# Kernel optimization log

Hardware: AMD Instinct MI355X
Metric: run time of the kernel (lower is better)

## Reference

```python
import jax, jax.numpy as jnp
import numpy as np
import math

B, H, L = 8, 512, 4096
N2 = 32  # d_state // 2


def setup_inputs() -> dict:
    key = jax.random.key(0)
    ks = jax.random.split(key, 8)
    u = jax.random.normal(ks[0], (B, H, L), dtype=jnp.float32)
    C = jax.random.normal(ks[1], (H, N2, 2), dtype=jnp.float32)  # view_as_real of cfloat C
    # log_dt ~ Uniform[log(dt_min), log(dt_max)], dt_min=1e-3, dt_max=0.1
    log_dt = jax.random.uniform(ks[2], (H,), dtype=jnp.float32,
                                minval=math.log(0.001), maxval=math.log(0.1))
    log_A_real = jnp.log(0.5 * jnp.ones((H, N2), dtype=jnp.float32))
    A_imag = math.pi * jnp.broadcast_to(jnp.arange(N2, dtype=jnp.float32), (H, N2))
    D = jax.random.normal(ks[3], (H,), dtype=jnp.float32)
    # pointwise Conv1d(H, 2H, kernel_size=1): weight (2H, H), bias (2H)
    fan = 1.0 / math.sqrt(H)
    W = jax.random.uniform(ks[4], (2 * H, H), dtype=jnp.float32, minval=-fan, maxval=fan)
    b = jax.random.uniform(ks[5], (2 * H,), dtype=jnp.float32, minval=-fan, maxval=fan)
    return {"u": u, "C": C, "log_dt": log_dt, "log_A_real": log_A_real,
            "A_imag": A_imag, "D": D, "W": W, "b": b}


def reference(u, C, log_dt, log_A_real, A_imag, D, W, b):
    Lb = u.shape[-1]
    # --- S4DKernel: kernel k of shape (H, L) ---
    dt = jnp.exp(log_dt)                                  # (H,)
    Cc = C[..., 0] + 1j * C[..., 1]                       # (H, N2) complex
    A = -jnp.exp(log_A_real) + 1j * A_imag                # (H, N2)
    dtA = A * dt[:, None]                                 # (H, N2)
    # Vandermonde: exp(dtA * l) for l in [0, L)
    K = jnp.exp(dtA[:, :, None] * jnp.arange(Lb, dtype=jnp.float32))  # (H, N2, L)
    Cmod = Cc * (jnp.exp(dtA) - 1.0) / A                  # (H, N2)
    k = 2.0 * jnp.einsum('hn,hnl->hl', Cmod, K).real      # (H, L)
    # --- FFT convolution (length 2L, causal) ---
    n = 2 * Lb
    k_f = jnp.fft.rfft(k, n=n)                            # (H, L+1)
    u_f = jnp.fft.rfft(u, n=n)                            # (B, H, L+1)
    y = jnp.fft.irfft(u_f * k_f, n=n)[..., :Lb]           # (B, H, L)
    # skip connection
    y = y + u * D[:, None]
    # activation (torch nn.GELU default = exact erf form)
    y = jax.nn.gelu(y, approximate=False)
    # pointwise conv (H -> 2H) + GLU over channel dim
    y = jnp.einsum('oh,bhl->bol', W, y) + b[None, :, None]  # (B, 2H, L)
    a, g = jnp.split(y, 2, axis=1)
    return a * jax.nn.sigmoid(g)                          # (B, H, L)
```

## Files before the change

### kernel.cpp

```cpp
#include <hip/hip_runtime.h>
#include <hip/hip_bf16.h>

constexpr int Bn = 8, Hn = 512, Ln = 4096, N2n = 32;

typedef _Float16 f16;
typedef __attribute__((ext_vector_type(8))) _Float16 f16x8;
typedef __attribute__((ext_vector_type(4))) _Float16 f16x4;
typedef __attribute__((ext_vector_type(2))) _Float16 f16x2;
typedef __attribute__((ext_vector_type(4))) float f32x4;

typedef void __attribute__((address_space(1))) gvoid;
typedef void __attribute__((address_space(3))) lvoid;

__global__ __launch_bounds__(64) void k_mats1(
    const float* __restrict__ C, const float* __restrict__ log_dt,
    const float* __restrict__ logA, const float* __restrict__ Aim,
    f16* __restrict__ Vg, f16* __restrict__ A3g, float2* __restrict__ w64g) {
  __shared__ f16 VT[64 * 64];
  __shared__ f16 QT[64 * 64];
  __shared__ float kp[64][33];
  __shared__ float ks[64];
  const int h = blockIdx.x, tid = threadIdx.x, n = tid & 31;

  if (tid < 32) {
    const int idx = h * N2n + n;
    float dt = expf(log_dt[h]);
    float Ar = -expf(logA[idx]);
    float Ai = Aim[idx];
    float dr = Ar * dt, di = Ai * dt;
    float er = expf(dr);
    float wr = er * cosf(di), wi = er * sinf(di);
    float den = Ar * Ar + Ai * Ai;
    float e1r = wr - 1.0f, e1i = wi;
    float tr = (e1r * Ar + e1i * Ai) / den;
    float ti = (e1i * Ar - e1r * Ai) / den;
    float Cr = C[idx * 2 + 0], Ci = C[idx * 2 + 1];
    float c2r = 2.0f * (Cr * tr - Ci * ti);
    float c2i = 2.0f * (Cr * ti + Ci * tr);

    float wpr = 1.f, wpi = 0.f;
    for (int p = 0; p <= 64; ++p) {
      float cwr = c2r * wpr - c2i * wpi;
      float cwi = c2r * wpi + c2i * wpr;
      if (p < 64) {
        const int j = 63 - p, ch = j >> 3, jo = j & 7;
        const int s0 = 2 * n, s1 = 2 * n + 1;
        VT[s0 * 64 + ((ch ^ (s0 & 7)) * 8) + jo] = (f16)wpr;
        VT[s1 * 64 + ((ch ^ (s1 & 7)) * 8) + jo] = (f16)wpi;
        kp[p][n] = cwr;
      }
      if (p >= 1) {
        const int t = p - 1, c0 = 2 * n;
        const int ch = (c0 >> 3) ^ (t & 7);
        QT[t * 64 + ch * 8 + (c0 & 7)]     = (f16)cwr;
        QT[t * 64 + ch * 8 + (c0 & 7) + 1] = (f16)(-cwi);
      }
      if (p == 64) w64g[h * 32 + n] = make_float2(wpr, wpi);
      float nr = wpr * wr - wpi * wi;
      float ni = wpr * wi + wpi * wr;
      wpr = nr; wpi = ni;
    }
  }
  __syncthreads();
  float s = 0.f;
#pragma unroll
  for (int m = 0; m < 32; ++m) s += kp[tid][m];
  ks[tid] = s;
  __syncthreads();
  const int t = tid;
#pragma unroll
  for (int c = 0; c < 8; ++c) {
    f16x8 row;
#pragma unroll
    for (int jo = 0; jo < 8; ++jo) {
      int j = c * 8 + jo;
      row[jo] = (j <= t) ? (f16)ks[t - j] : (f16)0.f;
    }
    *(f16x8*)&A3g[(size_t)h * 8192 + t * 128 + ((c ^ (t & 7)) * 8)] = row;
  }
#pragma unroll
  for (int c = 0; c < 8; ++c)
    *(f16x8*)&Vg[(size_t)h * 4096 + tid * 64 + c * 8] = *(f16x8*)&VT[tid * 64 + c * 8];
#pragma unroll
  for (int c = 0; c < 8; ++c)
    *(f16x8*)&A3g[(size_t)h * 8192 + tid * 128 + 64 + c * 8] = *(f16x8*)&QT[tid * 64 + c * 8];
}

__global__ void conv_w(const float* __restrict__ W, f16* __restrict__ Wh) {
  int i = blockIdx.x * 256 + threadIdx.x;
  if (i < 2 * Hn * Hn) Wh[i] = (f16)W[i];
}

__global__ __launch_bounds__(256, 1) void s4d_mid(
    const float* __restrict__ u, const f16* __restrict__ Vg,
    const f16* __restrict__ A3g, const float2* __restrict__ w64g,
    const float* __restrict__ Dv, f16* __restrict__ yg) {
  __shared__ f16 MATS[8192];
  __shared__ f16 U[32768];
  __shared__ f16 LE[32768];
  const int tid = threadIdx.x, wid = tid >> 6, lane = tid & 63;
  const int h = blockIdx.x;
  const float Dh = Dv[h];

#pragma unroll
  for (int q = 0; q < 2; ++q)
    __builtin_amdgcn_global_load_lds((const gvoid*)(Vg + (size_t)h * 4096 + (q * 256 + tid) * 8),
                                     (lvoid*)&MATS[(q * 256 + wid * 64) * 8], 16, 0, 0);
#pragma unroll
  for (int i = 0; i < 32; ++i) {
    int e = (i * 256 + tid) * 4;
    int b = e >> 12, l = e & 4095;
    float4 uv = *(const float4*)(u + ((size_t)(b * Hn + h)) * Ln + l);
    int col = b * 64 + (l >> 6), j = l & 63;
    f16x4 hv = {(f16)uv.x, (f16)uv.y, (f16)uv.z, (f16)uv.w};
    *(f16x4*)&U[col * 64 + ((j >> 3) ^ (col & 7)) * 8 + (j & 7)] = hv;
  }
  asm volatile("s_waitcnt vmcnt(0)" ::: "memory");
  __syncthreads();

  f32x4 acc[4][8];
#pragma unroll
  for (int i = 0; i < 4; ++i)
#pragma unroll
    for (int j = 0; j < 8; ++j) acc[i][j] = (f32x4){0.f, 0.f, 0.f, 0.f};
#pragma unroll
  for (int ks = 0; ks < 2; ++ks) {
    const int kc = ks * 4 + (lane >> 4);
    f16x8 a[4], bv[8];
#pragma unroll
    for (int mf = 0; mf < 4; ++mf) {
      int row = mf * 16 + (lane & 15);
      a[mf] = *(const f16x8*)&MATS[row * 64 + ((kc ^ (row & 7)) * 8)];
    }
#pragma unroll
    for (int nf = 0; nf < 8; ++nf) {
      int col = wid * 128 + nf * 16 + (lane & 15);
      bv[nf] = *(const f16x8*)&U[col * 64 + ((kc ^ (col & 7)) * 8)];
    }
#pragma unroll
    for (int mf = 0; mf < 4; ++mf)
#pragma unroll
      for (int nf = 0; nf < 8; ++nf)
        acc[mf][nf] = __builtin_amdgcn_mfma_f32_16x16x32_f16(a[mf], bv[nf], acc[mf][nf], 0, 0, 0);
  }
  __syncthreads();

#pragma unroll
  for (int q = 0; q < 4; ++q)
    __builtin_amdgcn_global_load_lds((const gvoid*)(A3g + (size_t)h * 8192 + (q * 256 + tid) * 8),
                                     (lvoid*)&MATS[(q * 256 + wid * 64) * 8], 16, 0, 0);

#pragma unroll
  for (int mf = 0; mf < 4; ++mf) {
    int st0 = mf * 16 + (lane >> 4) * 4;
#pragma unroll
    for (int nf = 0; nf < 8; ++nf) {
      int col = wid * 128 + nf * 16 + (lane & 15);
      f16x4 o = {(f16)acc[mf][nf][0], (f16)acc[mf][nf][1], (f16)acc[mf][nf][2], (f16)acc[mf][nf][3]};
      *(f16x4*)&LE[col * 64 + (((st0 >> 3) ^ (col & 7)) << 3) + (st0 & 7)] = o;
    }
  }
  __syncthreads();

  {
    const int b = tid >> 5, n = tid & 31;
    const float2 wT = w64g[h * 32 + n];
    float er = 0.f, ei = 0.f;
    const int inner = (((n >> 2)) << 3) + ((n & 3) << 1);
#pragma unroll
    for (int g = 0; g < 8; ++g) {
      f16x2 Lb[8];
#pragma unroll
      for (int k = 0; k < 8; ++k) {
        int blk = g * 8 + k;
        int col = b * 64 + blk;
        int fi = col * 64 + ((((n >> 2) ^ (blk & 7))) << 3) + ((n & 3) << 1);
        Lb[k] = *(const f16x2*)&LE[fi];
      }
#pragma unroll
      for (int k = 0; k < 8; ++k) {
        int blk = g * 8 + k;
        int col = b * 64 + blk;
        int fi = col * 64 + ((((n >> 2) ^ (blk & 7))) << 3) + ((n & 3) << 1);
        *(f16x2*)&LE[fi] = (f16x2){(f16)er, (f16)ei};
        float nr = fmaf(wT.x, er, fmaf(-wT.y, ei, (float)Lb[k][0]));
        float ni = fmaf(wT.y, er, fmaf(wT.x, ei, (float)Lb[k][1]));
        er = nr; ei = ni;
      }
    }
    (void)inner;
  }
  asm volatile("s_waitcnt vmcnt(0)" ::: "memory");
  __syncthreads();

  const int blk = wid * 16 + (lane & 15);
  for (int b = 0; b < 8; ++b) {
    const int col = b * 64 + blk;
    f32x4 acc4[4];
#pragma unroll
    for (int i = 0; i < 4; ++i) acc4[i] = (f32x4){0.f, 0.f, 0.f, 0.f};
#pragma unroll
    for (int ks = 0; ks < 4; ++ks) {
      const int kc = ks * 4 + (lane >> 4);
      f16x8 bf;
      if (ks < 2) bf = *(const f16x8*)&U[col * 64 + ((kc ^ (col & 7)) << 3)];
      else        bf = *(const f16x8*)&LE[col * 64 + (((kc - 8) ^ (col & 7)) << 3)];
#pragma unroll
      for (int mf = 0; mf < 4; ++mf) {
        int row = mf * 16 + (lane & 15);
        f16x8 af = *(const f16x8*)&MATS[row * 128 + ((kc ^ (row & 7)) << 3)];
        acc4[mf] = __builtin_amdgcn_mfma_f32_16x16x32_f16(af, bf, acc4[mf], 0, 0, 0);
      }
    }
    const int t0 = (lane >> 4) * 4;
#pragma unroll
    for (int mf = 0; mf < 4; ++mf) {
      const int tb = mf * 16 + t0;
      f16x4 uq = *(const f16x4*)&U[col * 64 + (((tb >> 3) ^ (col & 7)) << 3) + (tb & 7)];
      f16x4 o;
#pragma unroll
      for (int r = 0; r < 4; ++r) {
        float v = acc4[mf][r] + Dh * (float)uq[r];
        o[r] = (f16)(0.5f * v * (1.0f + erff(v * 0.70710678118654752f)));
      }
      *(f16x4*)&yg[((size_t)(b * Hn + h)) * Ln + blk * 64 + tb] = o;
    }
  }
}

__global__ __launch_bounds__(256) void k_transpose(
    const f16* __restrict__ yg, f16* __restrict__ gyT) {
  __shared__ float T[64][65];
  const int bid = blockIdx.x, tid = threadIdx.x;
  const int b = bid >> 9, hg = (bid >> 6) & 7, lg = bid & 63;
  const int h0 = hg * 64, l0 = lg * 64;
  const int hi = tid >> 2, lc = (tid & 3) * 16;
  const f16* src = yg + ((size_t)(b * Hn + h0 + hi)) * Ln + l0 + lc;
  f16x8 v0 = *(const f16x8*)src;
  f16x8 v1 = *(const f16x8*)(src + 8);
#pragma unroll
  for (int e = 0; e < 8; ++e) T[lc + e][hi] = (float)v0[e];
#pragma unroll
  for (int e = 0; e < 8; ++e) T[lc + 8 + e][hi] = (float)v1[e];
  __syncthreads();
  const int li = tid >> 2, hc = (tid & 3) * 16;
  f16x8 o0, o1;
#pragma unroll
  for (int e = 0; e < 8; ++e) o0[e] = (f16)T[li][hc + e];
#pragma unroll
  for (int e = 0; e < 8; ++e) o1[e] = (f16)T[li][hc + 8 + e];
  f16* dst = gyT + ((size_t)b * Ln + l0 + li) * Hn + h0 + hc;
  *(f16x8*)dst = o0;
  *(f16x8*)(dst + 8) = o1;
}

__global__ __launch_bounds__(256, 2) void s4d_gemm(
    const f16* __restrict__ Wh, const f16* __restrict__ gyT,
    const float* __restrict__ bias, float* __restrict__ out) {
  __shared__ f16 As[2][128][64];
  __shared__ f16 Bs[128][64];
  const int tid = threadIdx.x;
  const int wid = tid >> 6, lane = tid & 63;
  const int ntg = blockIdx.x & 255;
  const int mt = blockIdx.x >> 8;
  const int b = ntg >> 5;
  const int l0 = (ntg & 31) * 128;
  const int m0 = mt * 128;
  const int wm = wid >> 1, wn = wid & 1;

  f32x4 acc[2][4][4];
#pragma unroll
  for (int a = 0; a < 2; ++a)
#pragma unroll
    for (int i = 0; i < 4; ++i)
#pragma unroll
      for (int j = 0; j < 4; ++j) acc[a][i][j] = (f32x4){0.f, 0.f, 0.f, 0.f};

  const int srow = lane >> 3;
  const int sks = ((lane & 7) ^ srow) * 8;

  for (int kt = 0; kt < 8; ++kt) {
    const int k0 = kt * 64;
#pragma unroll
    for (int q = 0; q < 4; ++q) {
      const int r8 = wid * 32 + q * 8;
      const f16* srcA = Wh + ((size_t)(m0 + r8 + srow) * 512 + k0 + sks);
      __builtin_amdgcn_global_load_lds((const gvoid*)srcA, (lvoid*)&As[0][r8][0], 16, 0, 0);
      const f16* srcG = Wh + ((size_t)(Hn + m0 + r8 + srow) * 512 + k0 + sks);
      __builtin_amdgcn_global_load_lds((const gvoid*)srcG, (lvoid*)&As[1][r8][0], 16, 0, 0);
      const f16* srcB = gyT + (((size_t)b * Ln + l0 + r8 + srow) * Hn + k0 + sks);
      __builtin_amdgcn_global_load_lds((const gvoid*)srcB, (lvoid*)&Bs[r8][0], 16, 0, 0);
    }
    asm volatile("s_waitcnt vmcnt(0)" ::: "memory");
    __syncthreads();
#pragma unroll
    for (int kk = 0; kk < 2; ++kk) {
      const int kc = kk * 4 + (lane >> 4);
      f16x8 af0[4], af1[4], bfv[4];
#pragma unroll
      for (int mf = 0; mf < 4; ++mf) {
        const int row = wm * 64 + mf * 16 + (lane & 15);
        af0[mf] = *(const f16x8*)&As[0][row][(kc ^ (row & 7)) * 8];
        af1[mf] = *(const f16x8*)&As[1][row][(kc ^ (row & 7)) * 8];
      }
#pragma unroll
      for (int nf = 0; nf < 4; ++nf) {
        const int col = wn * 64 + nf * 16 + (lane & 15);
        bfv[nf] = *(const f16x8*)&Bs[col][(kc ^ (col & 7)) * 8];
      }
#pragma unroll
      for (int mf = 0; mf < 4; ++mf)
#pragma unroll
        for (int nf = 0; nf < 4; ++nf) {
          acc[0][mf][nf] = __builtin_amdgcn_mfma_f32_16x16x32_f16(af0[mf], bfv[nf], acc[0][mf][nf], 0, 0, 0);
          acc[1][mf][nf] = __builtin_amdgcn_mfma_f32_16x16x32_f16(af1[mf], bfv[nf], acc[1][mf][nf], 0, 0, 0);
        }
    }
    __syncthreads();
  }

  const int col = lane & 15, r0 = (lane >> 4) * 4;
#pragma unroll
  for (int mf = 0; mf < 4; ++mf) {
    const int hbase = m0 + wm * 64 + mf * 16 + r0;
#pragma unroll
    for (int nf = 0; nf < 4; ++nf) {
      const int l = l0 + wn * 64 + nf * 16 + col;
      f32x4 va = acc[0][mf][nf], vg = acc[1][mf][nf];
#pragma unroll
      for (int r = 0; r < 4; ++r) {
        const int hh = hbase + r;
        float av = va[r] + bias[hh];
        float gv = vg[r] + bias[Hn + hh];
        float sg = __builtin_amdgcn_rcpf(1.0f + __expf(-gv));
        out[((size_t)b * Hn + hh) * Ln + l] = av * sg;
      }
    }
  }
}

extern "C" void kernel_launch(void* const* d_in, const int* in_sizes, int n_in,
                              void* d_out, int out_size, void* d_ws, size_t ws_size,
                              hipStream_t stream) {
  (void)in_sizes; (void)n_in; (void)out_size; (void)ws_size;
  const float* u     = (const float*)d_in[0];
  const float* C     = (const float*)d_in[1];
  const float* logdt = (const float*)d_in[2];
  const float* logA  = (const float*)d_in[3];
  const float* Aim   = (const float*)d_in[4];
  const float* Dv    = (const float*)d_in[5];
  const float* W     = (const float*)d_in[6];
  const float* bias  = (const float*)d_in[7];
  float* out = (float*)d_out;

  char* ws = (char*)d_ws;
  f16*    gyT  = (f16*)ws;
  f16*    Vg   = (f16*)(ws + (size_t)(32 << 20));
  f16*    A3g  = (f16*)(ws + (size_t)(36 << 20));
  float2* w64g = (float2*)(ws + (size_t)(44 << 20));
  f16*    Wh   = (f16*)(ws + (size_t)(45 << 20));
  f16*    yg   = (f16*)d_out;

  hipLaunchKernelGGL(k_mats1, dim3(Hn), dim3(64), 0, stream, C, logdt, logA, Aim, Vg, A3g, w64g);
  hipLaunchKernelGGL(conv_w, dim3(2048), dim3(256), 0, stream, W, Wh);
  hipLaunchKernelGGL(s4d_mid, dim3(Hn), dim3(256), 0, stream, u, Vg, A3g, w64g, Dv, yg);
  hipLaunchKernelGGL(k_transpose, dim3(Bn * 8 * 64), dim3(256), 0, stream, yg, gyT);
  hipLaunchKernelGGL(s4d_gemm, dim3(4 * 256), dim3(256), 0, stream, Wh, gyT, bias, out);
}
```

Baseline: 120.4 us.

## Split s4d_mid grid across batch to shrink LDS and raise occupancy

The chunked scan kernel now launches one block per (head, batch) pair instead of one per head. Each block holds only one batch's 4096 samples, which cuts U/LE shared memory from 64 KB each to 8 KB each, and launch bounds now allow 4 blocks per CU. In exchange the per-head matrices (V, A3) are reloaded eight times. The inter-chunk recurrence also drops from 256 active threads to 32, which serialises that phase more within each block.

```diff
diff --git a/kernel.cpp b/kernel.cpp
--- a/kernel.cpp
+++ b/kernel.cpp
@@ -91,15 +91,15 @@
   if (i < 2 * Hn * Hn) Wh[i] = (f16)W[i];
 }
 
-__global__ __launch_bounds__(256, 1) void s4d_mid(
+__global__ __launch_bounds__(256, 4) void s4d_mid(
     const float* __restrict__ u, const f16* __restrict__ Vg,
     const f16* __restrict__ A3g, const float2* __restrict__ w64g,
     const float* __restrict__ Dv, f16* __restrict__ yg) {
   __shared__ f16 MATS[8192];
-  __shared__ f16 U[32768];
-  __shared__ f16 LE[32768];
+  __shared__ f16 U[4096];
+  __shared__ f16 LE[4096];
   const int tid = threadIdx.x, wid = tid >> 6, lane = tid & 63;
-  const int h = blockIdx.x;
+  const int h = blockIdx.x >> 3, b = blockIdx.x & 7;
   const float Dh = Dv[h];
 
 #pragma unroll
@@ -107,41 +107,30 @@
     __builtin_amdgcn_global_load_lds((const gvoid*)(Vg + (size_t)h * 4096 + (q * 256 + tid) * 8),
                                      (lvoid*)&MATS[(q * 256 + wid * 64) * 8], 16, 0, 0);
 #pragma unroll
-  for (int i = 0; i < 32; ++i) {
+  for (int i = 0; i < 4; ++i) {
     int e = (i * 256 + tid) * 4;
-    int b = e >> 12, l = e & 4095;
-    float4 uv = *(const float4*)(u + ((size_t)(b * Hn + h)) * Ln + l);
-    int col = b * 64 + (l >> 6), j = l & 63;
+    float4 uv = *(const float4*)(u + ((size_t)(b * Hn + h)) * Ln + e);
+    int col = e >> 6, j = e & 63;
     f16x4 hv = {(f16)uv.x, (f16)uv.y, (f16)uv.z, (f16)uv.w};
     *(f16x4*)&U[col * 64 + ((j >> 3) ^ (col & 7)) * 8 + (j & 7)] = hv;
   }
   asm volatile("s_waitcnt vmcnt(0)" ::: "memory");
   __syncthreads();
 
-  f32x4 acc[4][8];
-#pragma unroll
-  for (int i = 0; i < 4; ++i)
-#pragma unroll
-    for (int j = 0; j < 8; ++j) acc[i][j] = (f32x4){0.f, 0.f, 0.f, 0.f};
+  const int col = wid * 16 + (lane & 15);
+  f32x4 acc[4];
+#pragma unroll
+  for (int i = 0; i < 4; ++i) acc[i] = (f32x4){0.f, 0.f, 0.f, 0.f};
 #pragma unroll
   for (int ks = 0; ks < 2; ++ks) {
     const int kc = ks * 4 + (lane >> 4);
-    f16x8 a[4], bv[8];
+    f16x8 bv = *(const f16x8*)&U[col * 64 + ((kc ^ (col & 7)) * 8)];
 #pragma unroll
     for (int mf = 0; mf < 4; ++mf) {
       int row = mf * 16 + (lane & 15);
-      a[mf] = *(const f16x8*)&MATS[row * 64 + ((kc ^ (row & 7)) * 8)];
-    }
-#pragma unroll
-    for (int nf = 0; nf < 8; ++nf) {
-      int col = wid * 128 + nf * 16 + (lane & 15);
-      bv[nf] = *(const f16x8*)&U[col * 64 + ((kc ^ (col & 7)) * 8)];
-    }
-#pragma unroll
-    for (int mf = 0; mf < 4; ++mf)
-#pragma unroll
-      for (int nf = 0; nf < 8; ++nf)
-        acc[mf][nf] = __builtin_amdgcn_mfma_f32_16x16x32_f16(a[mf], bv[nf], acc[mf][nf], 0, 0, 0);
+      f16x8 a = *(const f16x8*)&MATS[row * 64 + ((kc ^ (row & 7)) * 8)];
+      acc[mf] = __builtin_amdgcn_mfma_f32_16x16x32_f16(a, bv, acc[mf], 0, 0, 0);
+    }
   }
   __syncthreads();
 
@@ -153,78 +142,66 @@
 #pragma unroll
   for (int mf = 0; mf < 4; ++mf) {
     int st0 = mf * 16 + (lane >> 4) * 4;
-#pragma unroll
-    for (int nf = 0; nf < 8; ++nf) {
-      int col = wid * 128 + nf * 16 + (lane & 15);
-      f16x4 o = {(f16)acc[mf][nf][0], (f16)acc[mf][nf][1], (f16)acc[mf][nf][2], (f16)acc[mf][nf][3]};
-      *(f16x4*)&LE[col * 64 + (((st0 >> 3) ^ (col & 7)) << 3) + (st0 & 7)] = o;
-    }
-  }
-  __syncthreads();
-
-  {
-    const int b = tid >> 5, n = tid & 31;
+    f16x4 o = {(f16)acc[mf][0], (f16)acc[mf][1], (f16)acc[mf][2], (f16)acc[mf][3]};
+    *(f16x4*)&LE[col * 64 + (((st0 >> 3) ^ (col & 7)) << 3) + (st0 & 7)] = o;
+  }
+  __syncthreads();
+
+  if (tid < 32) {
+    const int n = tid;
     const float2 wT = w64g[h * 32 + n];
     float er = 0.f, ei = 0.f;
-    const int inner = (((n >> 2)) << 3) + ((n & 3) << 1);
 #pragma unroll
     for (int g = 0; g < 8; ++g) {
       f16x2 Lb[8];
 #pragma unroll
       for (int k = 0; k < 8; ++k) {
         int blk = g * 8 + k;
-        int col = b * 64 + blk;
-        int fi = col * 64 + ((((n >> 2) ^ (blk & 7))) << 3) + ((n & 3) << 1);
+        int fi = blk * 64 + (((n >> 2) ^ (blk & 7)) << 3) + ((n & 3) << 1);
         Lb[k] = *(const f16x2*)&LE[fi];
       }
 #pragma unroll
       for (int k = 0; k < 8; ++k) {
         int blk = g * 8 + k;
-        int col = b * 64 + blk;
-        int fi = col * 64 + ((((n >> 2) ^ (blk & 7))) << 3) + ((n & 3) << 1);
+        int fi = blk * 64 + (((n >> 2) ^ (blk & 7)) << 3) + ((n & 3) << 1);
         *(f16x2*)&LE[fi] = (f16x2){(f16)er, (f16)ei};
         float nr = fmaf(wT.x, er, fmaf(-wT.y, ei, (float)Lb[k][0]));
         float ni = fmaf(wT.y, er, fmaf(wT.x, ei, (float)Lb[k][1]));
         er = nr; ei = ni;
       }
     }
-    (void)inner;
   }
   asm volatile("s_waitcnt vmcnt(0)" ::: "memory");
   __syncthreads();
 
-  const int blk = wid * 16 + (lane & 15);
-  for (int b = 0; b < 8; ++b) {
-    const int col = b * 64 + blk;
-    f32x4 acc4[4];
-#pragma unroll
-    for (int i = 0; i < 4; ++i) acc4[i] = (f32x4){0.f, 0.f, 0.f, 0.f};
-#pragma unroll
-    for (int ks = 0; ks < 4; ++ks) {
-      const int kc = ks * 4 + (lane >> 4);
-      f16x8 bf;
-      if (ks < 2) bf = *(const f16x8*)&U[col * 64 + ((kc ^ (col & 7)) << 3)];
-      else        bf = *(const f16x8*)&LE[col * 64 + (((kc - 8) ^ (col & 7)) << 3)];
-#pragma unroll
-      for (int mf = 0; mf < 4; ++mf) {
-        int row = mf * 16 + (lane & 15);
-        f16x8 af = *(const f16x8*)&MATS[row * 128 + ((kc ^ (row & 7)) << 3)];
-        acc4[mf] = __builtin_amdgcn_mfma_f32_16x16x32_f16(af, bf, acc4[mf], 0, 0, 0);
-      }
-    }
-    const int t0 = (lane >> 4) * 4;
+  f32x4 acc4[4];
+#pragma unroll
+  for (int i = 0; i < 4; ++i) acc4[i] = (f32x4){0.f, 0.f, 0.f, 0.f};
+#pragma unroll
+  for (int ks = 0; ks < 4; ++ks) {
+    const int kc = ks * 4 + (lane >> 4);
+    f16x8 bf;
+    if (ks < 2) bf = *(const f16x8*)&U[col * 64 + ((kc ^ (col & 7)) << 3)];
+    else        bf = *(const f16x8*)&LE[col * 64 + (((kc - 8) ^ (col & 7)) << 3)];
 #pragma unroll
     for (int mf = 0; mf < 4; ++mf) {
-      const int tb = mf * 16 + t0;
-      f16x4 uq = *(const f16x4*)&U[col * 64 + (((tb >> 3) ^ (col & 7)) << 3) + (tb & 7)];
-      f16x4 o;
-#pragma unroll
-      for (int r = 0; r < 4; ++r) {
-        float v = acc4[mf][r] + Dh * (float)uq[r];
-        o[r] = (f16)(0.5f * v * (1.0f + erff(v * 0.70710678118654752f)));
-      }
-      *(f16x4*)&yg[((size_t)(b * Hn + h)) * Ln + blk * 64 + tb] = o;
-    }
+      int row = mf * 16 + (lane & 15);
+      f16x8 af = *(const f16x8*)&MATS[row * 128 + ((kc ^ (row & 7)) << 3)];
+      acc4[mf] = __builtin_amdgcn_mfma_f32_16x16x32_f16(af, bf, acc4[mf], 0, 0, 0);
+    }
+  }
+  const int t0 = (lane >> 4) * 4;
+#pragma unroll
+  for (int mf = 0; mf < 4; ++mf) {
+    const int tb = mf * 16 + t0;
+    f16x4 uq = *(const f16x4*)&U[col * 64 + (((tb >> 3) ^ (col & 7)) << 3) + (tb & 7)];
+    f16x4 o;
+#pragma unroll
+    for (int r = 0; r < 4; ++r) {
+      float v = acc4[mf][r] + Dh * (float)uq[r];
+      o[r] = (f16)(0.5f * v * (1.0f + erff(v * 0.70710678118654752f)));
+    }
+    *(f16x4*)&yg[((size_t)(b * Hn + h)) * Ln + col * 64 + tb] = o;
   }
 }
 
@@ -363,7 +340,7 @@
 
   hipLaunchKernelGGL(k_mats1, dim3(Hn), dim3(64), 0, stream, C, logdt, logA, Aim, Vg, A3g, w64g);
   hipLaunchKernelGGL(conv_w, dim3(2048), dim3(256), 0, stream, W, Wh);
-  hipLaunchKernelGGL(s4d_mid, dim3(Hn), dim3(256), 0, stream, u, Vg, A3g, w64g, Dv, yg);
+  hipLaunchKernelGGL(s4d_mid, dim3(Hn * Bn), dim3(256), 0, stream, u, Vg, A3g, w64g, Dv, yg);
   hipLaunchKernelGGL(k_transpose, dim3(Bn * 8 * 64), dim3(256), 0, stream, yg, gyT);
   hipLaunchKernelGGL(s4d_gemm, dim3(4 * 256), dim3(256), 0, stream, Wh, gyT, bias, out);
 }
```

After: 112.5 us. 6.6% less time.
